# Kernel tuning notes

Measured on AMD Instinct MI355X. Metric: run time of the kernel, lower is better.

## Reference

```python
import jax, jax.numpy as jnp
import numpy as np

D_MODEL = 1024
N_HEADS = 16
D_K = D_MODEL // N_HEADS


def _rope_sin_cos(seq_len, d_k, dtype):
    inv_freq = 1.0 / (10000.0 ** (jnp.arange(0, d_k, 2, dtype=jnp.float32) / d_k))
    pos = jnp.arange(seq_len, dtype=jnp.float32)[:, None]          # [S,1]
    ang = pos * inv_freq[None, :]                                   # [S,d_k/2]
    sin = jnp.concatenate([jnp.sin(ang), jnp.sin(ang)], axis=-1)    # [S,d_k]
    cos = jnp.concatenate([jnp.cos(ang), jnp.cos(ang)], axis=-1)
    return sin.astype(dtype), cos.astype(dtype)


def _rotate_half(x):
    x1, x2 = jnp.split(x, 2, axis=-1)
    return jnp.concatenate([-x2, x1], axis=-1)


def _apply_rope(x, sin, cos):
    # x: [B,H,S,d_k]; sin/cos: [S,d_k] broadcast over B,H
    return x * cos[None, None] + _rotate_half(x) * sin[None, None]


def setup_inputs() -> dict:
    key = jax.random.key(0)
    ks = jax.random.split(key, 8)
    B, S = 2, 2048
    s = 1.0 / np.sqrt(D_MODEL)
    return {
        "query": jax.random.normal(ks[0], (B, S, D_MODEL), jnp.float32),
        "key": jax.random.normal(ks[1], (B, S, D_MODEL), jnp.float32),
        "value": jax.random.normal(ks[2], (B, S, D_MODEL), jnp.float32),
        "Wq": jax.random.normal(ks[3], (D_MODEL, D_MODEL), jnp.float32) * s,
        "Wk": jax.random.normal(ks[4], (D_MODEL, D_MODEL), jnp.float32) * s,
        "Wv": jax.random.normal(ks[5], (D_MODEL, D_MODEL), jnp.float32) * s,
        "Wo": jax.random.normal(ks[6], (D_MODEL, D_MODEL), jnp.float32) * s,
        "bo": jnp.zeros((D_MODEL,), jnp.float32),
    }


def reference(query, key, value, Wq, Wk, Wv, Wo, bo):
    B, Sq, _ = query.shape
    Sk = key.shape[1]
    # projections; torch Linear: x @ W.T (here W stored as [out,in])
    Q = (query @ Wq.T).reshape(B, Sq, N_HEADS, D_K).transpose(0, 2, 1, 3)
    K = (key @ Wk.T).reshape(B, Sk, N_HEADS, D_K).transpose(0, 2, 1, 3)
    V = (value @ Wv.T).reshape(B, Sk, N_HEADS, D_K).transpose(0, 2, 1, 3)
    sin_q, cos_q = _rope_sin_cos(Sq, D_K, Q.dtype)
    sin_k, cos_k = _rope_sin_cos(Sk, D_K, K.dtype)
    Q = _apply_rope(Q, sin_q, cos_q)
    K = _apply_rope(K, sin_k, cos_k)
    scores = jnp.einsum("bhqd,bhkd->bhqk", Q, K) / jnp.sqrt(jnp.asarray(D_K, Q.dtype))
    attn = jax.nn.softmax(scores, axis=-1)
    ctx = jnp.einsum("bhqk,bhkd->bhqd", attn, V)
    ctx = ctx.transpose(0, 2, 1, 3).reshape(B, Sq, D_MODEL)
    out = ctx @ Wo.T + bo
    return out, attn
```

## Files before the change

### kernel.cpp

```cpp
#include <hip/hip_runtime.h>
#include <cmath>

#define BB 2
#define SS 2048
#define DMODEL 1024
#define NHEADS 16
#define DK 64
#define BSR (BB*SS)

typedef float f32x4 __attribute__((ext_vector_type(4)));
typedef short s16x8 __attribute__((ext_vector_type(8)));
typedef unsigned short ushort_t;
#define MFMA_BF16 __builtin_amdgcn_mfma_f32_16x16x32_bf16

__device__ __forceinline__ unsigned short f2bf(float x) {
    unsigned int u = __float_as_uint(x);
    unsigned int r = u + 0x7FFFu + ((u >> 16) & 1u);
    return (unsigned short)(r >> 16);
}
__device__ __forceinline__ float bf2f(unsigned short h) {
    return __uint_as_float(((unsigned int)h) << 16);
}
__device__ __forceinline__ unsigned int pk2(float lo, float hi) {
    return (unsigned int)f2bf(lo) | ((unsigned int)f2bf(hi) << 16);
}

__device__ __forceinline__ size_t qk_idx(int bh, int s, int d) {
    return ((((size_t)bh * 128 + (s >> 4)) * 2 + (d >> 5)) * 4 + ((d >> 3) & 3)) * 128
           + (size_t)((s & 15) * 8 + (d & 7));
}
__device__ __forceinline__ size_t v_idx(int bh, int s, int d) {
    return ((((size_t)bh * 64 + (s >> 5)) * 4 + (d >> 4)) * 4 + ((s >> 3) & 3)) * 128
           + (size_t)((d & 15) * 8 + (s & 7));
}

__global__ __launch_bounds__(256)
void split_tab(const float* __restrict__ q, const float* __restrict__ k,
               const float* __restrict__ v, const float* __restrict__ wq,
               const float* __restrict__ wk, const float* __restrict__ wv,
               const float* __restrict__ wo,
               ushort_t* qsh, ushort_t* qsl, ushort_t* ksh, ushort_t* ksl,
               ushort_t* vsh, ushort_t* vsl,
               ushort_t* wqh, ushort_t* wql, ushort_t* wkh, ushort_t* wkl,
               ushort_t* wvh, ushort_t* wvl, ushort_t* woh, ushort_t* wol,
               float2* __restrict__ tab)
{
    int blk = blockIdx.x;
    if (blk >= 8192) {
        const int t = (blk - 8192) * 256 + threadIdx.x;
        const int s = t >> 5, j = t & 31;
        const double l2 = 13.287712379549449 / 32.0;
        const float invf = (float)exp2(-(double)j * l2);
        const float ang = (float)s * invf;
        tab[t] = make_float2(cosf(ang), sinf(ang));
        return;
    }
    const float* src; ushort_t* dh; ushort_t* dl;
    if      (blk < 2048) { src = q;  dh = qsh; dl = qsl; }
    else if (blk < 4096) { src = k;  dh = ksh; dl = ksl; blk -= 2048; }
    else if (blk < 6144) { src = v;  dh = vsh; dl = vsl; blk -= 4096; }
    else if (blk < 6656) { src = wq; dh = wqh; dl = wql; blk -= 6144; }
    else if (blk < 7168) { src = wk; dh = wkh; dl = wkl; blk -= 6656; }
    else if (blk < 7680) { src = wv; dh = wvh; dl = wvl; blk -= 7168; }
    else                 { src = wo; dh = woh; dl = wol; blk -= 7680; }
    const size_t off = (size_t)blk * 2048 + threadIdx.x * 8;
    float4 a = *reinterpret_cast<const float4*>(src + off);
    float4 b = *reinterpret_cast<const float4*>(src + off + 4);
    float xs[8] = {a.x, a.y, a.z, a.w, b.x, b.y, b.z, b.w};
    s16x8 hi, lo;
#pragma unroll
    for (int i = 0; i < 8; ++i) {
        unsigned short h = f2bf(xs[i]);
        hi[i] = (short)h;
        lo[i] = (short)f2bf(xs[i] - bf2f(h));
    }
    *reinterpret_cast<s16x8*>(dh + off) = hi;
    *reinterpret_cast<s16x8*>(dl + off) = lo;
}

__global__ __launch_bounds__(256)
void qkv_gemm(const ushort_t* __restrict__ qsh, const ushort_t* __restrict__ qsl,
              const ushort_t* __restrict__ ksh, const ushort_t* __restrict__ ksl,
              const ushort_t* __restrict__ vsh, const ushort_t* __restrict__ vsl,
              const ushort_t* __restrict__ wqh, const ushort_t* __restrict__ wql,
              const ushort_t* __restrict__ wkh, const ushort_t* __restrict__ wkl,
              const ushort_t* __restrict__ wvh, const ushort_t* __restrict__ wvl,
              ushort_t* __restrict__ Qhi, ushort_t* __restrict__ Qlo,
              ushort_t* __restrict__ Khi, ushort_t* __restrict__ Klo,
              ushort_t* __restrict__ Vt,
              const float2* __restrict__ tab)
{
    __shared__ __align__(16) ushort_t smAh[128 * 64];
    __shared__ __align__(16) ushort_t smAl[128 * 64];
    __shared__ __align__(16) ushort_t smBh[64 * 64];
    __shared__ __align__(16) ushort_t smBl[64 * 64];

    const int tid = threadIdx.x;
    const int lane = tid & 63;
    const int w = tid >> 6;
    const int lane16 = lane & 15;
    const int grp = (lane >> 4) & 3;
    const int m0 = blockIdx.y * 128;
    const int n0 = blockIdx.x * 64;
    const int z  = blockIdx.z;
    const int K = 1024;
    const bool split = (z != 0);

    const ushort_t* Ah = (z == 0) ? vsh : ((z == 1) ? qsh : ksh);
    const ushort_t* Al = (z == 0) ? vsl : ((z == 1) ? qsl : ksl);
    const ushort_t* Bh = (z == 0) ? wvh : ((z == 1) ? wqh : wkh);
    const ushort_t* Bl = (z == 0) ? wvl : ((z == 1) ? wql : wkl);

    f32x4 acc[2][4];
#pragma unroll
    for (int a = 0; a < 2; ++a)
#pragma unroll
        for (int e = 0; e < 4; ++e) acc[a][e] = (f32x4){0.f, 0.f, 0.f, 0.f};

    for (int k0 = 0; k0 < K; k0 += 64) {
#pragma unroll
        for (int i = 0; i < 4; ++i) {
            const int c = tid + 256 * i;
            const int row = c >> 3, gs = c & 7;
            const int dst = row * 64 + ((gs ^ (row & 7)) * 8);
            const size_t src = (size_t)(m0 + row) * K + k0 + gs * 8;
            *reinterpret_cast<s16x8*>(&smAh[dst]) = *reinterpret_cast<const s16x8*>(&Ah[src]);
            if (split)
                *reinterpret_cast<s16x8*>(&smAl[dst]) = *reinterpret_cast<const s16x8*>(&Al[src]);
        }
#pragma unroll
        for (int i = 0; i < 2; ++i) {
            const int c = tid + 256 * i;
            const int row = c >> 3, gs = c & 7;
            const int dst = row * 64 + ((gs ^ (row & 7)) * 8);
            const size_t src = (size_t)(n0 + row) * K + k0 + gs * 8;
            *reinterpret_cast<s16x8*>(&smBh[dst]) = *reinterpret_cast<const s16x8*>(&Bh[src]);
            if (split)
                *reinterpret_cast<s16x8*>(&smBl[dst]) = *reinterpret_cast<const s16x8*>(&Bl[src]);
        }
        __syncthreads();
#pragma unroll
        for (int ks = 0; ks < 2; ++ks) {
            const int slotk = ks * 4 + grp;
            s16x8 afh[2], afl[2], bfh[4], bfl[4];
#pragma unroll
            for (int mt = 0; mt < 2; ++mt) {
                const int row = w * 32 + mt * 16 + lane16;
                const int off = row * 64 + ((slotk ^ (row & 7)) * 8);
                afh[mt] = *reinterpret_cast<const s16x8*>(&smAh[off]);
                if (split) afl[mt] = *reinterpret_cast<const s16x8*>(&smAl[off]);
            }
#pragma unroll
            for (int nt = 0; nt < 4; ++nt) {
                const int row = nt * 16 + lane16;
                const int off = row * 64 + ((slotk ^ (row & 7)) * 8);
                bfh[nt] = *reinterpret_cast<const s16x8*>(&smBh[off]);
                if (split) bfl[nt] = *reinterpret_cast<const s16x8*>(&smBl[off]);
            }
#pragma unroll
            for (int mt = 0; mt < 2; ++mt)
#pragma unroll
                for (int nt = 0; nt < 4; ++nt) {
                    if (split) {
                        acc[mt][nt] = MFMA_BF16(afh[mt], bfl[nt], acc[mt][nt], 0, 0, 0);
                        acc[mt][nt] = MFMA_BF16(afl[mt], bfh[nt], acc[mt][nt], 0, 0, 0);
                    }
                    acc[mt][nt] = MFMA_BF16(afh[mt], bfh[nt], acc[mt][nt], 0, 0, 0);
                }
        }
        __syncthreads();
    }

    const int hh = blockIdx.x;
    if (z == 0) {
#pragma unroll
        for (int mt = 0; mt < 2; ++mt)
#pragma unroll
            for (int r = 0; r < 4; ++r) {
                const int m = m0 + w * 32 + mt * 16 + grp * 4 + r;
                const int b = m >> 11, s = m & (SS - 1);
                const int bh = b * 16 + hh;
#pragma unroll
                for (int nt = 0; nt < 4; ++nt) {
                    const int d = nt * 16 + lane16;
                    Vt[v_idx(bh, s, d)] = f2bf(acc[mt][nt][r]);
                }
            }
    } else {
        ushort_t* O1 = (z == 1) ? Qhi : Khi;
        ushort_t* O2 = (z == 1) ? Qlo : Klo;
#pragma unroll
        for (int mt = 0; mt < 2; ++mt)
#pragma unroll
            for (int r = 0; r < 4; ++r) {
                const int m = m0 + w * 32 + mt * 16 + grp * 4 + r;
                const int b = m >> 11, s = m & (SS - 1);
                const int bh = b * 16 + hh;
#pragma unroll
                for (int ntp = 0; ntp < 2; ++ntp) {
                    const int j = ntp * 16 + lane16;
                    const float2 cs = tab[s * 32 + j];
                    const float x1 = acc[mt][ntp][r], x2 = acc[mt][ntp + 2][r];
                    const float r1 = x1 * cs.x - x2 * cs.y;
                    const float r2 = x2 * cs.x + x1 * cs.y;
                    const size_t i1 = qk_idx(bh, s, j);
                    const size_t i2 = qk_idx(bh, s, j + 32);
                    const unsigned short h1 = f2bf(r1);
                    O1[i1] = h1;  O2[i1] = f2bf(r1 - bf2f(h1));
                    const unsigned short h2 = f2bf(r2);
                    O1[i2] = h2;  O2[i2] = f2bf(r2 - bf2f(h2));
                }
            }
    }
}

__global__ __launch_bounds__(256)
void gemm_out(const ushort_t* __restrict__ Ah, const ushort_t* __restrict__ Al,
              const ushort_t* __restrict__ Bh, const ushort_t* __restrict__ Bl,
              float* __restrict__ outF, const float* __restrict__ bias)
{
    __shared__ __align__(16) ushort_t smAh[128 * 64];
    __shared__ __align__(16) ushort_t smAl[128 * 64];
    __shared__ __align__(16) ushort_t smBh[64 * 64];
    __shared__ __align__(16) ushort_t smBl[64 * 64];

    const int tid = threadIdx.x;
    const int lane = tid & 63;
    const int w = tid >> 6;
    const int lane16 = lane & 15;
    const int grp = (lane >> 4) & 3;
    const int m0 = blockIdx.y * 128;
    const int n0 = blockIdx.x * 64;
    const int K = 1024;

    f32x4 acc[2][4];
#pragma unroll
    for (int a = 0; a < 2; ++a)
#pragma unroll
        for (int e = 0; e < 4; ++e) acc[a][e] = (f32x4){0.f, 0.f, 0.f, 0.f};

    for (int k0 = 0; k0 < K; k0 += 64) {
#pragma unroll
        for (int i = 0; i < 4; ++i) {
            const int c = tid + 256 * i;
            const int row = c >> 3, gs = c & 7;
            const int dst = row * 64 + ((gs ^ (row & 7)) * 8);
            const size_t src = (size_t)(m0 + row) * K + k0 + gs * 8;
            *reinterpret_cast<s16x8*>(&smAh[dst]) = *reinterpret_cast<const s16x8*>(&Ah[src]);
            *reinterpret_cast<s16x8*>(&smAl[dst]) = *reinterpret_cast<const s16x8*>(&Al[src]);
        }
#pragma unroll
        for (int i = 0; i < 2; ++i) {
            const int c = tid + 256 * i;
            const int row = c >> 3, gs = c & 7;
            const int dst = row * 64 + ((gs ^ (row & 7)) * 8);
            const size_t src = (size_t)(n0 + row) * K + k0 + gs * 8;
            *reinterpret_cast<s16x8*>(&smBh[dst]) = *reinterpret_cast<const s16x8*>(&Bh[src]);
            *reinterpret_cast<s16x8*>(&smBl[dst]) = *reinterpret_cast<const s16x8*>(&Bl[src]);
        }
        __syncthreads();
#pragma unroll
        for (int ks = 0; ks < 2; ++ks) {
            const int slotk = ks * 4 + grp;
            s16x8 afh[2], afl[2], bfh[4], bfl[4];
#pragma unroll
            for (int mt = 0; mt < 2; ++mt) {
                const int row = w * 32 + mt * 16 + lane16;
                const int off = row * 64 + ((slotk ^ (row & 7)) * 8);
                afh[mt] = *reinterpret_cast<const s16x8*>(&smAh[off]);
                afl[mt] = *reinterpret_cast<const s16x8*>(&smAl[off]);
            }
#pragma unroll
            for (int nt = 0; nt < 4; ++nt) {
                const int row = nt * 16 + lane16;
                const int off = row * 64 + ((slotk ^ (row & 7)) * 8);
                bfh[nt] = *reinterpret_cast<const s16x8*>(&smBh[off]);
                bfl[nt] = *reinterpret_cast<const s16x8*>(&smBl[off]);
            }
#pragma unroll
            for (int mt = 0; mt < 2; ++mt)
#pragma unroll
                for (int nt = 0; nt < 4; ++nt) {
                    acc[mt][nt] = MFMA_BF16(afh[mt], bfl[nt], acc[mt][nt], 0, 0, 0);
                    acc[mt][nt] = MFMA_BF16(afl[mt], bfh[nt], acc[mt][nt], 0, 0, 0);
                    acc[mt][nt] = MFMA_BF16(afh[mt], bfh[nt], acc[mt][nt], 0, 0, 0);
                }
        }
        __syncthreads();
    }

#pragma unroll
    for (int mt = 0; mt < 2; ++mt)
#pragma unroll
        for (int r = 0; r < 4; ++r) {
            const int m = m0 + w * 32 + mt * 16 + grp * 4 + r;
#pragma unroll
            for (int nt = 0; nt < 4; ++nt) {
                const int n = n0 + nt * 16 + lane16;
                outF[(size_t)m * 1024 + n] = acc[mt][nt][r] + bias[n];
            }
        }
}

#define SCALE_L2E 0.180336879f

__global__ __launch_bounds__(1024, 4)
void attn_v8(const ushort_t* __restrict__ Qf_h, const ushort_t* __restrict__ Qf_l,
             const ushort_t* __restrict__ Kf_h, const ushort_t* __restrict__ Kf_l,
             const ushort_t* __restrict__ Vf,
             float* __restrict__ attn, ushort_t* __restrict__ ctxh, ushort_t* __restrict__ ctxl)
{
    __shared__ __align__(16) float slots[8][32][68];
    __shared__ float lsum[16][32];
    __shared__ float rinvS[32];

    const int tid = threadIdx.x;
    const int lane = tid & 63;
    const int w = tid >> 6;
    const int lane16 = lane & 15;
    const int grp = lane >> 4;

    const int bid = blockIdx.x;
    const int idx = bid >> 3;
    const int bh = (bid & 7) * 4 + (idx >> 6);
    const int q0 = (idx & 63) * 32;

    s16x8 qh[2][2], ql[2][2];
#pragma unroll
    for (int qt = 0; qt < 2; ++qt) {
        const size_t qb = ((size_t)(bh * 128 + (q0 >> 4) + qt) * 2) * 512 + lane * 8;
        qh[qt][0] = *reinterpret_cast<const s16x8*>(Qf_h + qb);
        qh[qt][1] = *reinterpret_cast<const s16x8*>(Qf_h + qb + 512);
        ql[qt][0] = *reinterpret_cast<const s16x8*>(Qf_l + qb);
        ql[qt][1] = *reinterpret_cast<const s16x8*>(Qf_l + qb + 512);
    }

    unsigned int pp[8][2][2];
    float lq[2] = {0.f, 0.f};
#pragma unroll
    for (int kt = 0; kt < 8; ++kt) {
        const size_t kb = ((size_t)(bh * 128 + w * 8 + kt) * 2) * 512 + lane * 8;
        const s16x8 kh0 = *reinterpret_cast<const s16x8*>(Kf_h + kb);
        const s16x8 kh1 = *reinterpret_cast<const s16x8*>(Kf_h + kb + 512);
        const s16x8 kl0 = *reinterpret_cast<const s16x8*>(Kf_l + kb);
        const s16x8 kl1 = *reinterpret_cast<const s16x8*>(Kf_l + kb + 512);
#pragma unroll
        for (int qt = 0; qt < 2; ++qt) {
            f32x4 t = {0.f, 0.f, 0.f, 0.f};
            t = MFMA_BF16(kh0, ql[qt][0], t, 0, 0, 0);
            t = MFMA_BF16(kh1, ql[qt][1], t, 0, 0, 0);
            t = MFMA_BF16(kl0, qh[qt][0], t, 0, 0, 0);
            t = MFMA_BF16(kl1, qh[qt][1], t, 0, 0, 0);
            t = MFMA_BF16(kh0, qh[qt][0], t, 0, 0, 0);
            t = MFMA_BF16(kh1, qh[qt][1], t, 0, 0, 0);
            const float e0 = exp2f(t[0] * SCALE_L2E);
            const float e1 = exp2f(t[1] * SCALE_L2E);
            const float e2 = exp2f(t[2] * SCALE_L2E);
            const float e3 = exp2f(t[3] * SCALE_L2E);
            lq[qt] += e0 + e1 + e2 + e3;
            pp[kt][qt][0] = pk2(e0, e1);
            pp[kt][qt][1] = pk2(e2, e3);
        }
    }

#pragma unroll
    for (int qt = 0; qt < 2; ++qt) {
        lq[qt] += __shfl_xor(lq[qt], 16, 64);
        lq[qt] += __shfl_xor(lq[qt], 32, 64);
    }
    if (grp == 0) {
        lsum[w][lane16]      = lq[0];
        lsum[w][16 + lane16] = lq[1];
    }
    __syncthreads();
    float tot0 = 0.f, tot1 = 0.f;
#pragma unroll
    for (int w2 = 0; w2 < 16; ++w2) {
        tot0 += lsum[w2][lane16];
        tot1 += lsum[w2][16 + lane16];
    }
    const float rinv[2] = {1.0f / tot0, 1.0f / tot1};
    if (w == 0 && grp == 0) {
        rinvS[lane16]      = rinv[0];
        rinvS[16 + lane16] = rinv[1];
    }

#pragma unroll
    for (int qt = 0; qt < 2; ++qt) {
        const size_t arow = ((size_t)bh * SS + q0 + qt * 16 + lane16) * SS + w * 128 + grp * 4;
#pragma unroll
        for (int kt = 0; kt < 8; ++kt) {
            const unsigned int u0 = pp[kt][qt][0];
            const unsigned int u1 = pp[kt][qt][1];
            f32x4 v4;
            v4[0] = __uint_as_float(u0 << 16) * rinv[qt];
            v4[1] = __uint_as_float(u0 & 0xffff0000u) * rinv[qt];
            v4[2] = __uint_as_float(u1 << 16) * rinv[qt];
            v4[3] = __uint_as_float(u1 & 0xffff0000u) * rinv[qt];
            __builtin_nontemporal_store(v4, reinterpret_cast<f32x4*>(&attn[arow + kt * 16]));
        }
    }

    f32x4 acc[4][2];
#pragma unroll
    for (int dt = 0; dt < 4; ++dt) {
        acc[dt][0] = (f32x4){0.f, 0.f, 0.f, 0.f};
        acc[dt][1] = (f32x4){0.f, 0.f, 0.f, 0.f};
    }
    const int src0 = lane16 + ((grp & 1) << 5);
    const int src1 = src0 + 16;
    const bool sel = (grp >> 1) != 0;
#pragma unroll
    for (int kc = 0; kc < 4; ++kc) {
        s16x8 bfr[2];
#pragma unroll
        for (int qt = 0; qt < 2; ++qt) {
            const unsigned int A0 = pp[2 * kc][qt][0];
            const unsigned int A1 = pp[2 * kc][qt][1];
            const unsigned int B0 = pp[2 * kc + 1][qt][0];
            const unsigned int B1 = pp[2 * kc + 1][qt][1];
            const unsigned int d0a = (unsigned int)__shfl((int)A0, src0, 64);
            const unsigned int d0b = (unsigned int)__shfl((int)B0, src0, 64);
            const unsigned int d1a = (unsigned int)__shfl((int)A1, src0, 64);
            const unsigned int d1b = (unsigned int)__shfl((int)B1, src0, 64);
            const unsigned int d2a = (unsigned int)__shfl((int)A0, src1, 64);
            const unsigned int d2b = (unsigned int)__shfl((int)B0, src1, 64);
            const unsigned int d3a = (unsigned int)__shfl((int)A1, src1, 64);
            const unsigned int d3b = (unsigned int)__shfl((int)B1, src1, 64);
            union { unsigned int u[4]; s16x8 v; } bu;
            bu.u[0] = sel ? d0b : d0a;
            bu.u[1] = sel ? d1b : d1a;
            bu.u[2] = sel ? d2b : d2a;
            bu.u[3] = sel ? d3b : d3a;
            bfr[qt] = bu.v;
        }
#pragma unroll
        for (int dt = 0; dt < 4; ++dt) {
            const s16x8 vf = *reinterpret_cast<const s16x8*>(
                &Vf[((size_t)(bh * 64 + w * 4 + kc) * 4 + dt) * 512 + lane * 8]);
            acc[dt][0] = MFMA_BF16(vf, bfr[0], acc[dt][0], 0, 0, 0);
            acc[dt][1] = MFMA_BF16(vf, bfr[1], acc[dt][1], 0, 0, 0);
        }
    }

    if (w >= 8) {
        float* slot = &slots[w - 8][0][0];
#pragma unroll
        for (int dt = 0; dt < 4; ++dt)
#pragma unroll
            for (int qt = 0; qt < 2; ++qt) {
                f32x4 v4;
                v4[0] = acc[dt][qt][0]; v4[1] = acc[dt][qt][1];
                v4[2] = acc[dt][qt][2]; v4[3] = acc[dt][qt][3];
                *reinterpret_cast<f32x4*>(&slot[(qt * 16 + lane16) * 68 + dt * 16 + grp * 4]) = v4;
            }
    }
    __syncthreads();
    if (w < 8) {
        float* slot = &slots[w][0][0];
#pragma unroll
        for (int dt = 0; dt < 4; ++dt)
#pragma unroll
            for (int qt = 0; qt < 2; ++qt) {
                f32x4* pq = reinterpret_cast<f32x4*>(&slot[(qt * 16 + lane16) * 68 + dt * 16 + grp * 4]);
                f32x4 o = *pq;
                o[0] += acc[dt][qt][0]; o[1] += acc[dt][qt][1];
                o[2] += acc[dt][qt][2]; o[3] += acc[dt][qt][3];
                *pq = o;
            }
    }
    __syncthreads();

    {
        const int b = bh >> 4, h = bh & 15;
        const int q = tid >> 5;
        const int dp = (tid & 31) * 2;
        float s0 = 0.f, s1 = 0.f;
#pragma unroll
        for (int s = 0; s < 8; ++s) {
            const float2 v = *reinterpret_cast<const float2*>(&slots[s][q][dp]);
            s0 += v.x; s1 += v.y;
        }
        const float rv = rinvS[q];
        s0 *= rv; s1 *= rv;
        const size_t co = ((size_t)b * SS + q0 + q) * DMODEL + h * DK + dp;
        const unsigned short h0 = f2bf(s0);
        const unsigned short l0 = f2bf(s0 - bf2f(h0));
        const unsigned short h1 = f2bf(s1);
        const unsigned short l1 = f2bf(s1 - bf2f(h1));
        *reinterpret_cast<unsigned int*>(ctxh + co) = (unsigned int)h0 | ((unsigned int)h1 << 16);
        *reinterpret_cast<unsigned int*>(ctxl + co) = (unsigned int)l0 | ((unsigned int)l1 << 16);
    }
}

extern "C" void kernel_launch(void* const* d_in, const int* in_sizes, int n_in,
                              void* d_out, int out_size, void* d_ws, size_t ws_size,
                              hipStream_t stream)
{
    const float* query = (const float*)d_in[0];
    const float* key   = (const float*)d_in[1];
    const float* value = (const float*)d_in[2];
    const float* Wq    = (const float*)d_in[3];
    const float* Wk    = (const float*)d_in[4];
    const float* Wv    = (const float*)d_in[5];
    const float* Wo    = (const float*)d_in[6];
    const float* bo    = (const float*)d_in[7];

    float* out   = (float*)d_out;
    float* attnO = out + (size_t)BSR * DMODEL;

    const size_t NPROJ = (size_t)BSR * DMODEL;
    const size_t NW    = (size_t)DMODEL * DMODEL;

    char* p = (char*)d_ws;
    float2* tab = (float2*)p;                 p += 1 << 20;
    ushort_t* qsh = (ushort_t*)p;             p += NPROJ * 2;
    ushort_t* qsl = (ushort_t*)p;             p += NPROJ * 2;
    ushort_t* ksh = (ushort_t*)p;             p += NPROJ * 2;
    ushort_t* ksl = (ushort_t*)p;             p += NPROJ * 2;
    ushort_t* vsh = (ushort_t*)p;             p += NPROJ * 2;
    ushort_t* vsl = (ushort_t*)p;             p += NPROJ * 2;
    ushort_t* wqh = (ushort_t*)p;             p += NW * 2;
    ushort_t* wql = (ushort_t*)p;             p += NW * 2;
    ushort_t* wkh = (ushort_t*)p;             p += NW * 2;
    ushort_t* wkl = (ushort_t*)p;             p += NW * 2;
    ushort_t* wvh = (ushort_t*)p;             p += NW * 2;
    ushort_t* wvl = (ushort_t*)p;             p += NW * 2;
    ushort_t* woh = (ushort_t*)p;             p += NW * 2;
    ushort_t* wol = (ushort_t*)p;             p += NW * 2;
    ushort_t* Vt  = (ushort_t*)p;             p += NPROJ * 2;
    ushort_t* ctxhC = ksh;
    ushort_t* ctxlC = ksl;
    ushort_t* QhiX = (ushort_t*)p;            p += NPROJ * 2;
    ushort_t* QloX = (ushort_t*)p;            p += NPROJ * 2;
    ushort_t* KhiX = (ushort_t*)p;            p += NPROJ * 2;
    ushort_t* KloX = (ushort_t*)p;            p += NPROJ * 2;

    split_tab<<<8448, 256, 0, stream>>>(query, key, value, Wq, Wk, Wv, Wo,
                                        qsh, qsl, ksh, ksl, vsh, vsl,
                                        wqh, wql, wkh, wkl, wvh, wvl, woh, wol, tab);

    qkv_gemm<<<dim3(16, 32, 3), 256, 0, stream>>>(qsh, qsl, ksh, ksl, vsh, vsl,
                                                  wqh, wql, wkh, wkl, wvh, wvl,
                                                  QhiX, QloX, KhiX, KloX, Vt, tab);

    attn_v8<<<dim3(2048), 1024, 0, stream>>>(QhiX, QloX, KhiX, KloX, Vt, attnO, ctxhC, ctxlC);

    gemm_out<<<dim3(16, 32), 256, 0, stream>>>(ctxhC, ctxlC, woh, wol, out, bo);
}
```

Baseline: 339.0 us.

## Halve attention block size so each wave covers twice the key range

Result: slower. 373.0 us (+10.0%).

```diff
diff --git a/kernel.cpp b/kernel.cpp
--- a/kernel.cpp
+++ b/kernel.cpp
@@ -304,14 +304,14 @@
 
 #define SCALE_L2E 0.180336879f
 
-__global__ __launch_bounds__(1024, 4)
-void attn_v8(const ushort_t* __restrict__ Qf_h, const ushort_t* __restrict__ Qf_l,
+__global__ __launch_bounds__(512, 4)
+void attn_v9(const ushort_t* __restrict__ Qf_h, const ushort_t* __restrict__ Qf_l,
              const ushort_t* __restrict__ Kf_h, const ushort_t* __restrict__ Kf_l,
              const ushort_t* __restrict__ Vf,
              float* __restrict__ attn, ushort_t* __restrict__ ctxh, ushort_t* __restrict__ ctxl)
 {
     __shared__ __align__(16) float slots[8][32][68];
-    __shared__ float lsum[16][32];
+    __shared__ float lsum[8][32];
     __shared__ float rinvS[32];
 
     const int tid = threadIdx.x;
@@ -335,11 +335,11 @@
         ql[qt][1] = *reinterpret_cast<const s16x8*>(Qf_l + qb + 512);
     }
 
-    unsigned int pp[8][2][2];
+    unsigned int pp[16][2][2];
     float lq[2] = {0.f, 0.f};
 #pragma unroll
-    for (int kt = 0; kt < 8; ++kt) {
-        const size_t kb = ((size_t)(bh * 128 + w * 8 + kt) * 2) * 512 + lane * 8;
+    for (int kt = 0; kt < 16; ++kt) {
+        const size_t kb = ((size_t)(bh * 128 + w * 16 + kt) * 2) * 512 + lane * 8;
         const s16x8 kh0 = *reinterpret_cast<const s16x8*>(Kf_h + kb);
         const s16x8 kh1 = *reinterpret_cast<const s16x8*>(Kf_h + kb + 512);
         const s16x8 kl0 = *reinterpret_cast<const s16x8*>(Kf_l + kb);
@@ -375,7 +375,7 @@
     __syncthreads();
     float tot0 = 0.f, tot1 = 0.f;
 #pragma unroll
-    for (int w2 = 0; w2 < 16; ++w2) {
+    for (int w2 = 0; w2 < 8; ++w2) {
         tot0 += lsum[w2][lane16];
         tot1 += lsum[w2][16 + lane16];
     }
@@ -387,9 +387,9 @@
 
 #pragma unroll
     for (int qt = 0; qt < 2; ++qt) {
-        const size_t arow = ((size_t)bh * SS + q0 + qt * 16 + lane16) * SS + w * 128 + grp * 4;
-#pragma unroll
-        for (int kt = 0; kt < 8; ++kt) {
+        const size_t arow = ((size_t)bh * SS + q0 + qt * 16 + lane16) * SS + w * 256 + grp * 4;
+#pragma unroll
+        for (int kt = 0; kt < 16; ++kt) {
             const unsigned int u0 = pp[kt][qt][0];
             const unsigned int u1 = pp[kt][qt][1];
             f32x4 v4;
@@ -411,7 +411,7 @@
     const int src1 = src0 + 16;
     const bool sel = (grp >> 1) != 0;
 #pragma unroll
-    for (int kc = 0; kc < 4; ++kc) {
+    for (int kc = 0; kc < 8; ++kc) {
         s16x8 bfr[2];
 #pragma unroll
         for (int qt = 0; qt < 2; ++qt) {
@@ -437,59 +437,47 @@
 #pragma unroll
         for (int dt = 0; dt < 4; ++dt) {
             const s16x8 vf = *reinterpret_cast<const s16x8*>(
-                &Vf[((size_t)(bh * 64 + w * 4 + kc) * 4 + dt) * 512 + lane * 8]);
+                &Vf[((size_t)(bh * 64 + w * 8 + kc) * 4 + dt) * 512 + lane * 8]);
             acc[dt][0] = MFMA_BF16(vf, bfr[0], acc[dt][0], 0, 0, 0);
             acc[dt][1] = MFMA_BF16(vf, bfr[1], acc[dt][1], 0, 0, 0);
         }
     }
 
-    if (w >= 8) {
-        float* slot = &slots[w - 8][0][0];
-#pragma unroll
-        for (int dt = 0; dt < 4; ++dt)
-#pragma unroll
-            for (int qt = 0; qt < 2; ++qt) {
-                f32x4 v4;
-                v4[0] = acc[dt][qt][0]; v4[1] = acc[dt][qt][1];
-                v4[2] = acc[dt][qt][2]; v4[3] = acc[dt][qt][3];
-                *reinterpret_cast<f32x4*>(&slot[(qt * 16 + lane16) * 68 + dt * 16 + grp * 4]) = v4;
-            }
-    }
-    __syncthreads();
-    if (w < 8) {
-        float* slot = &slots[w][0][0];
-#pragma unroll
-        for (int dt = 0; dt < 4; ++dt)
-#pragma unroll
-            for (int qt = 0; qt < 2; ++qt) {
-                f32x4* pq = reinterpret_cast<f32x4*>(&slot[(qt * 16 + lane16) * 68 + dt * 16 + grp * 4]);
-                f32x4 o = *pq;
-                o[0] += acc[dt][qt][0]; o[1] += acc[dt][qt][1];
-                o[2] += acc[dt][qt][2]; o[3] += acc[dt][qt][3];
-                *pq = o;
-            }
-    }
+#pragma unroll
+    for (int dt = 0; dt < 4; ++dt)
+#pragma unroll
+        for (int qt = 0; qt < 2; ++qt) {
+            f32x4 v4;
+            v4[0] = acc[dt][qt][0]; v4[1] = acc[dt][qt][1];
+            v4[2] = acc[dt][qt][2]; v4[3] = acc[dt][qt][3];
+            *reinterpret_cast<f32x4*>(&slots[w][qt * 16 + lane16][dt * 16 + grp * 4]) = v4;
+        }
     __syncthreads();
 
     {
         const int b = bh >> 4, h = bh & 15;
-        const int q = tid >> 5;
-        const int dp = (tid & 31) * 2;
-        float s0 = 0.f, s1 = 0.f;
-#pragma unroll
-        for (int s = 0; s < 8; ++s) {
-            const float2 v = *reinterpret_cast<const float2*>(&slots[s][q][dp]);
-            s0 += v.x; s1 += v.y;
+        const int q = tid >> 4;
+        const int dp = (tid & 15) * 4;
+        f32x4 s = {0.f, 0.f, 0.f, 0.f};
+#pragma unroll
+        for (int sl = 0; sl < 8; ++sl) {
+            const f32x4 v = *reinterpret_cast<const f32x4*>(&slots[sl][q][dp]);
+            s[0] += v[0]; s[1] += v[1]; s[2] += v[2]; s[3] += v[3];
         }
         const float rv = rinvS[q];
-        s0 *= rv; s1 *= rv;
         const size_t co = ((size_t)b * SS + q0 + q) * DMODEL + h * DK + dp;
-        const unsigned short h0 = f2bf(s0);
-        const unsigned short l0 = f2bf(s0 - bf2f(h0));
-        const unsigned short h1 = f2bf(s1);
-        const unsigned short l1 = f2bf(s1 - bf2f(h1));
-        *reinterpret_cast<unsigned int*>(ctxh + co) = (unsigned int)h0 | ((unsigned int)h1 << 16);
-        *reinterpret_cast<unsigned int*>(ctxl + co) = (unsigned int)l0 | ((unsigned int)l1 << 16);
+        const unsigned short h0 = f2bf(s[0] * rv);
+        const unsigned short h1 = f2bf(s[1] * rv);
+        const unsigned short h2 = f2bf(s[2] * rv);
+        const unsigned short h3 = f2bf(s[3] * rv);
+        const unsigned short l0 = f2bf(s[0] * rv - bf2f(h0));
+        const unsigned short l1 = f2bf(s[1] * rv - bf2f(h1));
+        const unsigned short l2 = f2bf(s[2] * rv - bf2f(h2));
+        const unsigned short l3 = f2bf(s[3] * rv - bf2f(h3));
+        *reinterpret_cast<unsigned int*>(ctxh + co)     = (unsigned int)h0 | ((unsigned int)h1 << 16);
+        *reinterpret_cast<unsigned int*>(ctxh + co + 2) = (unsigned int)h2 | ((unsigned int)h3 << 16);
+        *reinterpret_cast<unsigned int*>(ctxl + co)     = (unsigned int)l0 | ((unsigned int)l1 << 16);
+        *reinterpret_cast<unsigned int*>(ctxl + co + 2) = (unsigned int)l2 | ((unsigned int)l3 << 16);
     }
 }
 
@@ -544,7 +532,7 @@
                                                   wqh, wql, wkh, wkl, wvh, wvl,
                                                   QhiX, QloX, KhiX, KloX, Vt, tab);
 
-    attn_v8<<<dim3(2048), 1024, 0, stream>>>(QhiX, QloX, KhiX, KloX, Vt, attnO, ctxhC, ctxlC);
+    attn_v9<<<dim3(2048), 512, 0, stream>>>(QhiX, QloX, KhiX, KloX, Vt, attnO, ctxhC, ctxlC);
 
     gemm_out<<<dim3(16, 32), 256, 0, stream>>>(ctxhC, ctxlC, woh, wol, out, bo);
 }
```

## Restructure attention kernel to 16-query blocks with 8 waves covering 256 keys each

Applied to the files above, without the earlier changes.

Result: slower. 347.5 us (+2.5%).

```diff
diff --git a/kernel.cpp b/kernel.cpp
--- a/kernel.cpp
+++ b/kernel.cpp
@@ -304,15 +304,15 @@
 
 #define SCALE_L2E 0.180336879f
 
-__global__ __launch_bounds__(1024, 4)
-void attn_v8(const ushort_t* __restrict__ Qf_h, const ushort_t* __restrict__ Qf_l,
-             const ushort_t* __restrict__ Kf_h, const ushort_t* __restrict__ Kf_l,
-             const ushort_t* __restrict__ Vf,
-             float* __restrict__ attn, ushort_t* __restrict__ ctxh, ushort_t* __restrict__ ctxl)
+__global__ __launch_bounds__(512, 4)
+void attn_v10(const ushort_t* __restrict__ Qf_h, const ushort_t* __restrict__ Qf_l,
+              const ushort_t* __restrict__ Kf_h, const ushort_t* __restrict__ Kf_l,
+              const ushort_t* __restrict__ Vf,
+              float* __restrict__ attn, ushort_t* __restrict__ ctxh, ushort_t* __restrict__ ctxl)
 {
-    __shared__ __align__(16) float slots[8][32][68];
-    __shared__ float lsum[16][32];
-    __shared__ float rinvS[32];
+    __shared__ __align__(16) float slots[8][16][68];
+    __shared__ float lsum[8][16];
+    __shared__ float rinvS[16];
 
     const int tid = threadIdx.x;
     const int lane = tid & 63;
@@ -322,155 +322,104 @@
 
     const int bid = blockIdx.x;
     const int idx = bid >> 3;
-    const int bh = (bid & 7) * 4 + (idx >> 6);
-    const int q0 = (idx & 63) * 32;
-
-    s16x8 qh[2][2], ql[2][2];
-#pragma unroll
-    for (int qt = 0; qt < 2; ++qt) {
-        const size_t qb = ((size_t)(bh * 128 + (q0 >> 4) + qt) * 2) * 512 + lane * 8;
-        qh[qt][0] = *reinterpret_cast<const s16x8*>(Qf_h + qb);
-        qh[qt][1] = *reinterpret_cast<const s16x8*>(Qf_h + qb + 512);
-        ql[qt][0] = *reinterpret_cast<const s16x8*>(Qf_l + qb);
-        ql[qt][1] = *reinterpret_cast<const s16x8*>(Qf_l + qb + 512);
-    }
-
-    unsigned int pp[8][2][2];
-    float lq[2] = {0.f, 0.f};
-#pragma unroll
-    for (int kt = 0; kt < 8; ++kt) {
-        const size_t kb = ((size_t)(bh * 128 + w * 8 + kt) * 2) * 512 + lane * 8;
+    const int bh = (bid & 7) * 4 + (idx >> 7);
+    const int q0 = (idx & 127) * 16;
+
+    const size_t qb = ((size_t)(bh * 128 + (q0 >> 4)) * 2) * 512 + lane * 8;
+    const s16x8 qh0 = *reinterpret_cast<const s16x8*>(Qf_h + qb);
+    const s16x8 qh1 = *reinterpret_cast<const s16x8*>(Qf_h + qb + 512);
+    const s16x8 ql0 = *reinterpret_cast<const s16x8*>(Qf_l + qb);
+    const s16x8 ql1 = *reinterpret_cast<const s16x8*>(Qf_l + qb + 512);
+
+    unsigned int pp[16][2];
+    float lq = 0.f;
+#pragma unroll
+    for (int kt = 0; kt < 16; ++kt) {
+        const size_t kb = ((size_t)(bh * 128 + w * 16 + kt) * 2) * 512 + lane * 8;
         const s16x8 kh0 = *reinterpret_cast<const s16x8*>(Kf_h + kb);
         const s16x8 kh1 = *reinterpret_cast<const s16x8*>(Kf_h + kb + 512);
         const s16x8 kl0 = *reinterpret_cast<const s16x8*>(Kf_l + kb);
         const s16x8 kl1 = *reinterpret_cast<const s16x8*>(Kf_l + kb + 512);
-#pragma unroll
-        for (int qt = 0; qt < 2; ++qt) {
-            f32x4 t = {0.f, 0.f, 0.f, 0.f};
-            t = MFMA_BF16(kh0, ql[qt][0], t, 0, 0, 0);
-            t = MFMA_BF16(kh1, ql[qt][1], t, 0, 0, 0);
-            t = MFMA_BF16(kl0, qh[qt][0], t, 0, 0, 0);
-            t = MFMA_BF16(kl1, qh[qt][1], t, 0, 0, 0);
-            t = MFMA_BF16(kh0, qh[qt][0], t, 0, 0, 0);
-            t = MFMA_BF16(kh1, qh[qt][1], t, 0, 0, 0);
-            const float e0 = exp2f(t[0] * SCALE_L2E);
-            const float e1 = exp2f(t[1] * SCALE_L2E);
-            const float e2 = exp2f(t[2] * SCALE_L2E);
-            const float e3 = exp2f(t[3] * SCALE_L2E);
-            lq[qt] += e0 + e1 + e2 + e3;
-            pp[kt][qt][0] = pk2(e0, e1);
-            pp[kt][qt][1] = pk2(e2, e3);
-        }
-    }
-
-#pragma unroll
-    for (int qt = 0; qt < 2; ++qt) {
-        lq[qt] += __shfl_xor(lq[qt], 16, 64);
-        lq[qt] += __shfl_xor(lq[qt], 32, 64);
-    }
-    if (grp == 0) {
-        lsum[w][lane16]      = lq[0];
-        lsum[w][16 + lane16] = lq[1];
-    }
+        f32x4 t = {0.f, 0.f, 0.f, 0.f};
+        t = MFMA_BF16(kh0, ql0, t, 0, 0, 0);
+        t = MFMA_BF16(kh1, ql1, t, 0, 0, 0);
+        t = MFMA_BF16(kl0, qh0, t, 0, 0, 0);
+        t = MFMA_BF16(kl1, qh1, t, 0, 0, 0);
+        t = MFMA_BF16(kh0, qh0, t, 0, 0, 0);
+        t = MFMA_BF16(kh1, qh1, t, 0, 0, 0);
+        const float e0 = exp2f(t[0] * SCALE_L2E);
+        const float e1 = exp2f(t[1] * SCALE_L2E);
+        const float e2 = exp2f(t[2] * SCALE_L2E);
+        const float e3 = exp2f(t[3] * SCALE_L2E);
+        lq += e0 + e1 + e2 + e3;
+        pp[kt][0] = pk2(e0, e1);
+        pp[kt][1] = pk2(e2, e3);
+    }
+
+    lq += __shfl_xor(lq, 16, 64);
+    lq += __shfl_xor(lq, 32, 64);
+    if (grp == 0) lsum[w][lane16] = lq;
     __syncthreads();
-    float tot0 = 0.f, tot1 = 0.f;
-#pragma unroll
-    for (int w2 = 0; w2 < 16; ++w2) {
-        tot0 += lsum[w2][lane16];
-        tot1 += lsum[w2][16 + lane16];
-    }
-    const float rinv[2] = {1.0f / tot0, 1.0f / tot1};
-    if (w == 0 && grp == 0) {
-        rinvS[lane16]      = rinv[0];
-        rinvS[16 + lane16] = rinv[1];
-    }
-
-#pragma unroll
-    for (int qt = 0; qt < 2; ++qt) {
-        const size_t arow = ((size_t)bh * SS + q0 + qt * 16 + lane16) * SS + w * 128 + grp * 4;
-#pragma unroll
-        for (int kt = 0; kt < 8; ++kt) {
-            const unsigned int u0 = pp[kt][qt][0];
-            const unsigned int u1 = pp[kt][qt][1];
-            f32x4 v4;
-            v4[0] = __uint_as_float(u0 << 16) * rinv[qt];
-            v4[1] = __uint_as_float(u0 & 0xffff0000u) * rinv[qt];
-            v4[2] = __uint_as_float(u1 << 16) * rinv[qt];
-            v4[3] = __uint_as_float(u1 & 0xffff0000u) * rinv[qt];
-            __builtin_nontemporal_store(v4, reinterpret_cast<f32x4*>(&attn[arow + kt * 16]));
-        }
-    }
-
-    f32x4 acc[4][2];
-#pragma unroll
-    for (int dt = 0; dt < 4; ++dt) {
-        acc[dt][0] = (f32x4){0.f, 0.f, 0.f, 0.f};
-        acc[dt][1] = (f32x4){0.f, 0.f, 0.f, 0.f};
-    }
+    float tot = 0.f;
+#pragma unroll
+    for (int w2 = 0; w2 < 8; ++w2) tot += lsum[w2][lane16];
+    const float rinv = 1.0f / tot;
+    if (tid < 16) rinvS[tid] = rinv;
+
+    const size_t arow = ((size_t)bh * SS + q0 + lane16) * SS + w * 256 + grp * 4;
+#pragma unroll
+    for (int kt = 0; kt < 16; ++kt) {
+        const unsigned int u0 = pp[kt][0];
+        const unsigned int u1 = pp[kt][1];
+        f32x4 v4;
+        v4[0] = __uint_as_float(u0 << 16) * rinv;
+        v4[1] = __uint_as_float(u0 & 0xffff0000u) * rinv;
+        v4[2] = __uint_as_float(u1 << 16) * rinv;
+        v4[3] = __uint_as_float(u1 & 0xffff0000u) * rinv;
+        __builtin_nontemporal_store(v4, reinterpret_cast<f32x4*>(&attn[arow + kt * 16]));
+    }
+
+    f32x4 acc[4];
+#pragma unroll
+    for (int dt = 0; dt < 4; ++dt) acc[dt] = (f32x4){0.f, 0.f, 0.f, 0.f};
     const int src0 = lane16 + ((grp & 1) << 5);
     const int src1 = src0 + 16;
     const bool sel = (grp >> 1) != 0;
 #pragma unroll
-    for (int kc = 0; kc < 4; ++kc) {
-        s16x8 bfr[2];
-#pragma unroll
-        for (int qt = 0; qt < 2; ++qt) {
-            const unsigned int A0 = pp[2 * kc][qt][0];
-            const unsigned int A1 = pp[2 * kc][qt][1];
-            const unsigned int B0 = pp[2 * kc + 1][qt][0];
-            const unsigned int B1 = pp[2 * kc + 1][qt][1];
-            const unsigned int d0a = (unsigned int)__shfl((int)A0, src0, 64);
-            const unsigned int d0b = (unsigned int)__shfl((int)B0, src0, 64);
-            const unsigned int d1a = (unsigned int)__shfl((int)A1, src0, 64);
-            const unsigned int d1b = (unsigned int)__shfl((int)B1, src0, 64);
-            const unsigned int d2a = (unsigned int)__shfl((int)A0, src1, 64);
-            const unsigned int d2b = (unsigned int)__shfl((int)B0, src1, 64);
-            const unsigned int d3a = (unsigned int)__shfl((int)A1, src1, 64);
-            const unsigned int d3b = (unsigned int)__shfl((int)B1, src1, 64);
-            union { unsigned int u[4]; s16x8 v; } bu;
-            bu.u[0] = sel ? d0b : d0a;
-            bu.u[1] = sel ? d1b : d1a;
-            bu.u[2] = sel ? d2b : d2a;
-            bu.u[3] = sel ? d3b : d3a;
-            bfr[qt] = bu.v;
-        }
+    for (int kc = 0; kc < 8; ++kc) {
+        const unsigned int A0 = pp[2 * kc][0];
+        const unsigned int A1 = pp[2 * kc][1];
+        const unsigned int B0 = pp[2 * kc + 1][0];
+        const unsigned int B1 = pp[2 * kc + 1][1];
+        const unsigned int d0a = (unsigned int)__shfl((int)A0, src0, 64);
+        const unsigned int d0b = (unsigned int)__shfl((int)B0, src0, 64);
+        const unsigned int d1a = (unsigned int)__shfl((int)A1, src0, 64);
+        const unsigned int d1b = (unsigned int)__shfl((int)B1, src0, 64);
+        const unsigned int d2a = (unsigned int)__shfl((int)A0, src1, 64);
+        const unsigned int d2b = (unsigned int)__shfl((int)B0, src1, 64);
+        const unsigned int d3a = (unsigned int)__shfl((int)A1, src1, 64);
+        const unsigned int d3b = (unsigned int)__shfl((int)B1, src1, 64);
+        union { unsigned int u[4]; s16x8 v; } bu;
+        bu.u[0] = sel ? d0b : d0a;
+        bu.u[1] = sel ? d1b : d1a;
+        bu.u[2] = sel ? d2b : d2a;
+        bu.u[3] = sel ? d3b : d3a;
 #pragma unroll
         for (int dt = 0; dt < 4; ++dt) {
             const s16x8 vf = *reinterpret_cast<const s16x8*>(
-                &Vf[((size_t)(bh * 64 + w * 4 + kc) * 4 + dt) * 512 + lane * 8]);
-            acc[dt][0] = MFMA_BF16(vf, bfr[0], acc[dt][0], 0, 0, 0);
-            acc[dt][1] = MFMA_BF16(vf, bfr[1], acc[dt][1], 0, 0, 0);
-        }
-    }
-
-    if (w >= 8) {
-        float* slot = &slots[w - 8][0][0];
-#pragma unroll
-        for (int dt = 0; dt < 4; ++dt)
-#pragma unroll
-            for (int qt = 0; qt < 2; ++qt) {
-                f32x4 v4;
-                v4[0] = acc[dt][qt][0]; v4[1] = acc[dt][qt][1];
-                v4[2] = acc[dt][qt][2]; v4[3] = acc[dt][qt][3];
-                *reinterpret_cast<f32x4*>(&slot[(qt * 16 + lane16) * 68 + dt * 16 + grp * 4]) = v4;
-            }
+                &Vf[((size_t)(bh * 64 + w * 8 + kc) * 4 + dt) * 512 + lane * 8]);
+            acc[dt] = MFMA_BF16(vf, bu.v, acc[dt], 0, 0, 0);
+        }
+    }
+
+#pragma unroll
+    for (int dt = 0; dt < 4; ++dt) {
+        f32x4 v4;
+        v4[0] = acc[dt][0]; v4[1] = acc[dt][1];
+        v4[2] = acc[dt][2]; v4[3] = acc[dt][3];
+        *reinterpret_cast<f32x4*>(&slots[w][lane16][dt * 16 + grp * 4]) = v4;
     }
     __syncthreads();
-    if (w < 8) {
-        float* slot = &slots[w][0][0];
-#pragma unroll
-        for (int dt = 0; dt < 4; ++dt)
-#pragma unroll
-            for (int qt = 0; qt < 2; ++qt) {
-                f32x4* pq = reinterpret_cast<f32x4*>(&slot[(qt * 16 + lane16) * 68 + dt * 16 + grp * 4]);
-                f32x4 o = *pq;
-                o[0] += acc[dt][qt][0]; o[1] += acc[dt][qt][1];
-                o[2] += acc[dt][qt][2]; o[3] += acc[dt][qt][3];
-                *pq = o;
-            }
-    }
-    __syncthreads();
-
     {
         const int b = bh >> 4, h = bh & 15;
         const int q = tid >> 5;
@@ -544,7 +493,7 @@
                                                   wqh, wql, wkh, wkl, wvh, wvl,
                                                   QhiX, QloX, KhiX, KloX, Vt, tab);
 
-    attn_v8<<<dim3(2048), 1024, 0, stream>>>(QhiX, QloX, KhiX, KloX, Vt, attnO, ctxhC, ctxlC);
+    attn_v10<<<dim3(4096), 512, 0, stream>>>(QhiX, QloX, KhiX, KloX, Vt, attnO, ctxhC, ctxlC);
 
     gemm_out<<<dim3(16, 32), 256, 0, stream>>>(ctxhC, ctxlC, woh, wol, out, bo);
 }
```
